# Performance work log

Measured on AMD Instinct MI355X. Metric: run time of the kernel, lower is better.

Reference implementation:

```python
import jax, jax.numpy as jnp
import numpy as np

N_OBJ, N_REL = 2048, 32768
OBJ_DIM, POOL, H, E, C = 4096, 2048, 512, 200, 151
GEO = 128
IMG_W, IMG_H = 1024.0, 768.0
NUM_ITER = 3


def _lin(x, W, b):
    return x @ W.T + b


def _gru(x, h, Wih, Whh, bih, bhh):
    # torch.nn.GRUCell math; gates stacked (r, z, n)
    gi = x @ Wih.T + bih
    gh = h @ Whh.T + bhh
    i_r, i_z, i_n = jnp.split(gi, 3, axis=-1)
    h_r, h_z, h_n = jnp.split(gh, 3, axis=-1)
    r = jax.nn.sigmoid(i_r + h_r)
    z = jax.nn.sigmoid(i_z + h_z)
    n = jnp.tanh(i_n + r * h_n)
    return (1.0 - z) * n + z * h


def _box_info(boxes, norm=None):
    # [x1,y1,x2,y2,cx,cy,w,h]
    wh = boxes[:, 2:4] - boxes[:, 0:2] + 1.0
    ctr = boxes[:, 0:2] + 0.5 * wh
    info = jnp.concatenate([boxes, ctr, wh], axis=1)
    return info / norm if norm is not None else info


def _box_pair_info(b1, b2):
    # b1,b2: [R,8] normalized box infos -> [R,32]
    ub = jnp.stack([jnp.minimum(b1[:, 0], b2[:, 0]), jnp.minimum(b1[:, 1], b2[:, 1]),
                    jnp.maximum(b1[:, 2], b2[:, 2]), jnp.maximum(b1[:, 3], b2[:, 3])], axis=1)
    ib = jnp.stack([jnp.maximum(b1[:, 0], b2[:, 0]), jnp.maximum(b1[:, 1], b2[:, 1]),
                    jnp.minimum(b1[:, 2], b2[:, 2]), jnp.minimum(b1[:, 3], b2[:, 3])], axis=1)
    inter = _box_info(ib)
    bad = (ib[:, 2] < ib[:, 0]) | (ib[:, 3] < ib[:, 1])
    inter = jnp.where(bad[:, None], 0.0, inter)
    return jnp.concatenate([b1, b2, _box_info(ub), inter], axis=1)


def _encode_box_info(boxes):
    # motifs 9-d geometry encoding
    wh = boxes[:, 2:4] - boxes[:, 0:2] + 1.0
    xy = boxes[:, 0:2] + 0.5 * wh
    w, h = wh[:, 0:1], wh[:, 1:2]
    x, y = xy[:, 0:1], xy[:, 1:2]
    x1, y1, x2, y2 = boxes[:, 0:1], boxes[:, 1:2], boxes[:, 2:3], boxes[:, 3:4]
    return jnp.concatenate([w / IMG_W, h / IMG_H, x / IMG_W, y / IMG_H, x1 / IMG_W,
                            y1 / IMG_H, x2 / IMG_W, y2 / IMG_H, w * h / (IMG_W * IMG_H)], axis=1)


def _forward(inst_roi_feats, union_features, boxes, emb_dist_W, emb_label_W, up_W, up_b,
             pairup_W, pairup_b, pos1_W, pos1_b, bn_g, bn_b, bn_m, bn_v, pos2_W, pos2_b,
             spt1_W, spt1_b, spt2_W, spt2_b, pairfin_W, pairfin_b, objhid_W, objhid_b,
             objfin_W, objfin_b, objU_W, objU_b, edgeU_W, edgeU_b,
             egru_Wih, egru_Whh, egru_bih, egru_bhh, ngru_Wih, ngru_Whh, ngru_bih, ngru_bhh,
             svw_W, svw_b, ovw_W, ovw_b, obj_labels, sub_idx, obj_idx):
    # ---- PairwiseFeatureExtractor ----
    # pos_embed: fc(9,32) -> eval BatchNorm1d(32) -> fc(32,128) -> ReLU
    p = _lin(_encode_box_info(boxes), pos1_W, pos1_b)
    p = (p - bn_m) * bn_g / jnp.sqrt(bn_v + 1e-5) + bn_b
    pos_embed = jax.nn.relu(_lin(p, pos2_W, pos2_b))
    emb_dist = emb_dist_W[obj_labels]                       # predcls: embed GT labels
    aug = _lin(jnp.concatenate([inst_roi_feats, emb_dist, pos_embed], 1), objhid_W, objhid_b)
    augment = jnp.concatenate([emb_label_W[obj_labels], inst_roi_feats, aug], 1)  # [N,4808]
    # pairwise (edge) features: gather head/tail reps + spatial gating
    obox = _box_info(boxes, norm=max(IMG_W, IMG_H, 100.0))  # [N,8]
    fused = _lin(augment, pairup_W, pairup_b).reshape(-1, 2, H)
    pair = jnp.concatenate([fused[:, 0][sub_idx], fused[:, 1][obj_idx]], 1)  # [R,1024]
    geo = _box_pair_info(obox[sub_idx], obox[obj_idx])      # [R,32]
    spt = jax.nn.relu(_lin(jax.nn.relu(_lin(geo, spt1_W, spt1_b)), spt2_W, spt2_b))
    rel_feats = jax.nn.relu(_lin(pair * spt, pairfin_W, pairfin_b))
    rel_feats = rel_feats + _lin(union_features, up_W, up_b)  # 'fusion' + dim-up
    obj_feats = jax.nn.relu(_lin(augment, objfin_W, objfin_b))
    # ---- IMP iterative message passing ----
    obj_rep = _lin(obj_feats, objU_W, objU_b)
    rel_rep = jax.nn.relu(_lin(rel_feats, edgeU_W, edgeU_b))
    vert = _gru(obj_rep, jnp.zeros_like(obj_rep), ngru_Wih, ngru_Whh, ngru_bih, ngru_bhh)
    edge = _gru(rel_rep, jnp.zeros_like(rel_rep), egru_Wih, egru_Whh, egru_bih, egru_bhh)
    n = vert.shape[0]
    for _ in range(NUM_ITER):
        sv, ov = vert[sub_idx], vert[obj_idx]
        ws = jax.nn.sigmoid(_lin(jnp.concatenate([sv, edge], 1), svw_W, svw_b))  # [R,1]
        wo = jax.nn.sigmoid(_lin(jnp.concatenate([ov, edge], 1), ovw_W, ovw_b))
        new_edge = _gru(ws * sv + wo * ov, edge, egru_Wih, egru_Whh, egru_bih, egru_bhh)
        # sub2rel @ (ws*edge) + obj2rel @ (wo*edge) == segment sums over pair indices
        ctx = jax.ops.segment_sum(ws * edge, sub_idx, n) + jax.ops.segment_sum(wo * edge, obj_idx, n)
        vert = _gru(ctx, vert, ngru_Wih, ngru_Whh, ngru_bih, ngru_bhh)
        edge = new_edge
    return vert, edge


def setup_inputs() -> dict:
    keys = jax.random.split(jax.random.key(0), 64)
    ki = iter(keys)

    def nrm(shape, s=0.02):
        return (jax.random.normal(next(ki), shape) * s).astype(jnp.float32)

    kb = jax.random.split(next(ki), 4)
    x1 = jax.random.uniform(kb[0], (N_OBJ,)) * (IMG_W - 200.0)
    y1 = jax.random.uniform(kb[1], (N_OBJ,)) * (IMG_H - 150.0)
    x2 = x1 + 1.0 + jax.random.uniform(kb[2], (N_OBJ,)) * 199.0
    y2 = y1 + 1.0 + jax.random.uniform(kb[3], (N_OBJ,)) * 149.0
    boxes = jnp.stack([x1, y1, x2, y2], axis=1).astype(jnp.float32)

    inp = {
        'inst_roi_feats': nrm((N_OBJ, OBJ_DIM), 1.0),
        'union_features': nrm((N_REL, OBJ_DIM), 1.0),
        'boxes': boxes,
        'emb_dist_W': nrm((C, E)), 'emb_label_W': nrm((C, E)),
        'up_W': nrm((POOL, OBJ_DIM)), 'up_b': jnp.zeros((POOL,), jnp.float32),
        'pairup_W': nrm((2 * H, H + OBJ_DIM + E)), 'pairup_b': jnp.zeros((2 * H,), jnp.float32),
        'pos1_W': nrm((32, 9)), 'pos1_b': jnp.zeros((32,), jnp.float32),
        'bn_g': jnp.ones((32,), jnp.float32), 'bn_b': jnp.zeros((32,), jnp.float32),
        'bn_m': nrm((32,)), 'bn_v': jnp.ones((32,), jnp.float32),
        'pos2_W': nrm((GEO, 32)), 'pos2_b': jnp.zeros((GEO,), jnp.float32),
        'spt1_W': nrm((H, 32)), 'spt1_b': jnp.zeros((H,), jnp.float32),
        'spt2_W': nrm((2 * H, H)), 'spt2_b': jnp.zeros((2 * H,), jnp.float32),
        'pairfin_W': nrm((POOL, 2 * H)), 'pairfin_b': jnp.zeros((POOL,), jnp.float32),
        'objhid_W': nrm((H, OBJ_DIM + E + GEO)), 'objhid_b': jnp.zeros((H,), jnp.float32),
        'objfin_W': nrm((POOL, H + OBJ_DIM + E)), 'objfin_b': jnp.zeros((POOL,), jnp.float32),
        'objU_W': nrm((H, POOL)), 'objU_b': jnp.zeros((H,), jnp.float32),
        'edgeU_W': nrm((H, POOL)), 'edgeU_b': jnp.zeros((H,), jnp.float32),
        'egru_Wih': nrm((3 * H, H)), 'egru_Whh': nrm((3 * H, H)),
        'egru_bih': jnp.zeros((3 * H,), jnp.float32), 'egru_bhh': jnp.zeros((3 * H,), jnp.float32),
        'ngru_Wih': nrm((3 * H, H)), 'ngru_Whh': nrm((3 * H, H)),
        'ngru_bih': jnp.zeros((3 * H,), jnp.float32), 'ngru_bhh': jnp.zeros((3 * H,), jnp.float32),
        'svw_W': nrm((1, 2 * H)), 'svw_b': jnp.zeros((1,), jnp.float32),
        'ovw_W': nrm((1, 2 * H)), 'ovw_b': jnp.zeros((1,), jnp.float32),
        'obj_labels': jax.random.randint(next(ki), (N_OBJ,), 0, C),
        'sub_idx': jax.random.randint(next(ki), (N_REL,), 0, N_OBJ),
        'obj_idx': jax.random.randint(next(ki), (N_REL,), 0, N_OBJ),
    }
    return inp


def reference(inst_roi_feats, union_features, boxes, emb_dist_W, emb_label_W, up_W, up_b,
              pairup_W, pairup_b, pos1_W, pos1_b, bn_g, bn_b, bn_m, bn_v, pos2_W, pos2_b,
              spt1_W, spt1_b, spt2_W, spt2_b, pairfin_W, pairfin_b, objhid_W, objhid_b,
              objfin_W, objfin_b, objU_W, objU_b, edgeU_W, edgeU_b,
              egru_Wih, egru_Whh, egru_bih, egru_bhh, ngru_Wih, ngru_Whh, ngru_bih, ngru_bhh,
              svw_W, svw_b, ovw_W, ovw_b, obj_labels, sub_idx, obj_idx):
    return _forward(inst_roi_feats, union_features, boxes, emb_dist_W, emb_label_W, up_W, up_b,
                    pairup_W, pairup_b, pos1_W, pos1_b, bn_g, bn_b, bn_m, bn_v, pos2_W, pos2_b,
                    spt1_W, spt1_b, spt2_W, spt2_b, pairfin_W, pairfin_b, objhid_W, objhid_b,
                    objfin_W, objfin_b, objU_W, objU_b, edgeU_W, edgeU_b,
                    egru_Wih, egru_Whh, egru_bih, egru_bhh, ngru_Wih, ngru_Whh, ngru_bih, ngru_bhh,
                    svw_W, svw_b, ovw_W, ovw_b, obj_labels, sub_idx, obj_idx)
```

## Files before the change

kernel.cpp:

```cpp
#include <hip/hip_runtime.h>
#include <stdint.h>

#define NOBJ 2048
#define NREL 32768

typedef __attribute__((ext_vector_type(8))) short short8;
typedef __attribute__((ext_vector_type(4))) float f32x4;
typedef __attribute__((ext_vector_type(4))) unsigned short ushort4v;

__device__ __forceinline__ unsigned short f2bs(float x){
  unsigned u = __float_as_uint(x);
  unsigned v = u + 0x7fffu + ((u >> 16) & 1u);
  return (unsigned short)(v >> 16);
}
__device__ __forceinline__ float b2f(unsigned short u){
  return __uint_as_float(((unsigned)u) << 16);
}
__device__ __forceinline__ float sigf(float x){ return 1.0f / (1.0f + expf(-x)); }

__device__ __forceinline__ void gload16(const unsigned short* g, unsigned short* l) {
  __builtin_amdgcn_global_load_lds(
      (const __attribute__((address_space(1))) unsigned int*)(uintptr_t)g,
      (__attribute__((address_space(3))) unsigned int*)(uintptr_t)l,
      16, 0, 0);
// ... 220 lines not shown
    asm volatile("" ::: "memory");
    __builtin_amdgcn_s_barrier();
    asm volatile("" ::: "memory");
    if (kt + 2 < NT) stage(cur, kt + 2);
  }

#pragma unroll
  for (int i = 0; i < 2; i++) {
#pragma unroll
    for (int j = 0; j < 2; j++) {
      const int col = n0 + wn + j * 16 + lrow;
      const float bv = bias[col];
#pragma unroll
      for (int q = 0; q < 4; q++) {
        const long row = m0 + wm + i * 16 + kg * 4 + q;
        float v = acc[i][j][q] + bv;
        if constexpr (RMODE == 1) v = fmaxf(v, 0.0f);
        C[row * (long)ldc + col] = f2bs(v);
      }
    }
  }
}


__global__ void cvt_pad4(const float* __restrict__ src, unsigned short* __restrict__ dst,
                         int rows, int K0, int Kp)
{
  const int kp4 = Kp >> 2;
  const long total = (long)rows * kp4;
  for (long i = blockIdx.x * (long)blockDim.x + threadIdx.x; i < total; i += (long)gridDim.x * blockDim.x) {
    int r = (int)(i / kp4), k = (int)(i - (long)r * kp4) << 2;
    ushort4v o;
    if (k < K0) {
      f32x4 v = *(const f32x4*)(src + (long)r * K0 + k);
      o[0] = f2bs(v[0]); o[1] = f2bs(v[1]); o[2] = f2bs(v[2]); o[3] = f2bs(v[3]);
    } else {
      o[0] = 0; o[1] = 0; o[2] = 0; o[3] = 0;
    }
    *(ushort4v*)(dst + (long)r * Kp + k) = o;
  }
}

struct CvtSeg { const float* src; unsigned short* dst; long base; long n4; };
struct Cvt9 { CvtSeg s[9]; long total; };

__global__ void cvt4_multi(Cvt9 cfg)
{
  for (long i = blockIdx.x * (long)blockDim.x + threadIdx.x; i < cfg.total;
       i += (long)gridDim.x * blockDim.x) {
#pragma unroll
    for (int k = 0; k < 9; k++) {
      if (i >= cfg.s[k].base && i < cfg.s[k].base + cfg.s[k].n4) {
        long j = i - cfg.s[k].base;
        f32x4 v = ((const f32x4*)cfg.s[k].src)[j];
        ushort4v o;
        o[0] = f2bs(v[0]); o[1] = f2bs(v[1]); o[2] = f2bs(v[2]); o[3] = f2bs(v[3]);
        ((ushort4v*)cfg.s[k].dst)[j] = o;
        break;
      }
    }
  }
}

__global__ void transpose_cvt(const float* __restrict__ src, unsigned short* __restrict__ dst,
                              int R, int C)
{
  __shared__ float tile[32][33];
  int c0 = blockIdx.x * 32, r0 = blockIdx.y * 32;
  for (int i = threadIdx.y; i < 32; i += 8)
    tile[i][threadIdx.x] = src[(long)(r0 + i) * C + c0 + threadIdx.x];
  __syncthreads();
  for (int i = threadIdx.y; i < 32; i += 8)
    dst[(long)(c0 + i) * R + r0 + threadIdx.x] = f2bs(tile[threadIdx.x][i]);
}

__global__ void comp_bias(const float* __restrict__ edgeU_W, const float* __restrict__ up_b,
                          const float* __restrict__ edgeU_b, float* __restrict__ b_comp)
{
  int j = (int)((blockIdx.x * (long)blockDim.x + threadIdx.x) >> 6);
  int l = threadIdx.x & 63;
  if (j >= 512) return;
  float s = 0.0f;
  for (int k = l; k < 2048; k += 64) s += edgeU_W[(long)j * 2048 + k] * up_b[k];
#pragma unroll
  for (int off = 32; off > 0; off >>= 1) s += __shfl_xor(s, off);
  if (l == 0) b_comp[j] = s + edgeU_b[j];
}

__global__ void bias_cat(const float* __restrict__ bhh, float* __restrict__ out)
{
  int j = blockIdx.x * blockDim.x + threadIdx.x;
  if (j < 3072) out[j] = (j < 1536) ? 0.0f : bhh[j - 1536];
}

__global__ void obox_k(const float* __restrict__ boxes, float* __restrict__ obox)
{
  int i = blockIdx.x * blockDim.x + threadIdx.x;
  if (i >= NOBJ) return;
  float x1 = boxes[i*4], y1 = boxes[i*4+1], x2 = boxes[i*4+2], y2 = boxes[i*4+3];
  float wdt = x2 - x1 + 1.0f, hgt = y2 - y1 + 1.0f;
  float cx = x1 + 0.5f * wdt, cy = y1 + 0.5f * hgt;
  const float inv = 1.0f / 1024.0f;
  float* o = obox + i * 8;
  o[0]=x1*inv; o[1]=y1*inv; o[2]=x2*inv; o[3]=y2*inv;
  o[4]=cx*inv; o[5]=cy*inv; o[6]=wdt*inv; o[7]=hgt*inv;
}

__global__ void posembed_k(const float* __restrict__ boxes,
                           const float* __restrict__ w1, const float* __restrict__ b1,
                           const float* __restrict__ g, const float* __restrict__ bb,
                           const float* __restrict__ mm, const float* __restrict__ vv,
                           const float* __restrict__ w2, const float* __restrict__ b2,
                           float* __restrict__ out)
{
  int o = blockIdx.x, t = threadIdx.x;
  __shared__ float e[9];
  __shared__ float p[32];
  if (t == 0) {
    float x1 = boxes[o*4], y1 = boxes[o*4+1], x2 = boxes[o*4+2], y2 = boxes[o*4+3];
    float wdt = x2 - x1 + 1.0f, hgt = y2 - y1 + 1.0f;
    float cx = x1 + 0.5f * wdt, cy = y1 + 0.5f * hgt;
    e[0]=wdt/1024.0f; e[1]=hgt/768.0f; e[2]=cx/1024.0f; e[3]=cy/768.0f;
    e[4]=x1/1024.0f;  e[5]=y1/768.0f;  e[6]=x2/1024.0f; e[7]=y2/768.0f;
    e[8]=wdt*hgt/(1024.0f*768.0f);
  }
  __syncthreads();
  if (t < 32) {
    float s = b1[t];
#pragma unroll
    for (int j = 0; j < 9; j++) s += w1[t*9+j] * e[j];
    s = (s - mm[t]) * g[t] / sqrtf(vv[t] + 1e-5f) + bb[t];
    p[t] = s;
  }
  __syncthreads();
  float s = b2[t];
#pragma unroll
  for (int j = 0; j < 32; j++) s += w2[t*32+j] * p[j];
  out[o*128 + t] = fmaxf(s, 0.0f);
}

__device__ __forceinline__ void pack8_store(unsigned short* dst, f32x4 a, f32x4 b)
{
  ushort4v o0, o1;
  o0[0]=f2bs(a[0]); o0[1]=f2bs(a[1]); o0[2]=f2bs(a[2]); o0[3]=f2bs(a[3]);
  o1[0]=f2bs(b[0]); o1[1]=f2bs(b[1]); o1[2]=f2bs(b[2]); o1[3]=f2bs(b[3]);
  *(ushort4v*)dst = o0;
  *(ushort4v*)(dst + 4) = o1;
}

__global__ void build_x1(const float* __restrict__ inst, const float* __restrict__ embd,
                         const int* __restrict__ labels, const float* __restrict__ pose,
                         unsigned short* __restrict__ X1b)
{
  const long total = (long)NOBJ * 560;
  for (long i = blockIdx.x * (long)blockDim.x + threadIdx.x; i < total; i += (long)gridDim.x * blockDim.x) {
    int r = (int)(i / 560), c = ((int)(i - (long)r * 560)) << 3;
    unsigned short* dst = X1b + (long)r * 4480 + c;
    const float* src;
    if (c < 4096)      src = inst + (long)r * 4096 + c;
    else if (c < 4296) src = embd + (long)labels[r] * 200 + (c - 4096);
    else if (c < 4424) src = pose + r * 128 + (c - 4296);
    else { ushort4v z = {0,0,0,0}; *(ushort4v*)dst = z; *(ushort4v*)(dst+4) = z; continue; }
    pack8_store(dst, *(const f32x4*)src, *((const f32x4*)src + 1));
  }
}

__global__ void build_aug(const float* __restrict__ embl, const int* __restrict__ labels,
                          const float* __restrict__ inst, unsigned short* __restrict__ augb)
{
  const long total = (long)NOBJ * 608;
  for (long i = blockIdx.x * (long)blockDim.x + threadIdx.x; i < total; i += (long)gridDim.x * blockDim.x) {
    int r = (int)(i / 608), c = ((int)(i - (long)r * 608)) << 3;
    if (c >= 4296 && c < 4808) continue;
    unsigned short* dst = augb + (long)r * 4864 + c;
    const float* src;
    if (c < 200)       src = embl + (long)labels[r] * 200 + c;
    else if (c < 4296) src = inst + (long)r * 4096 + (c - 200);
    else { ushort4v z = {0,0,0,0}; *(ushort4v*)dst = z; *(ushort4v*)(dst+4) = z; continue; }
    pack8_store(dst, *(const f32x4*)src, *((const f32x4*)src + 1));
  }
}

__global__ void build_geo(const float* __restrict__ obox, const int* __restrict__ sub,
                          const int* __restrict__ obj, unsigned short* __restrict__ geob)
{
  int r = blockIdx.x * blockDim.x + threadIdx.x;
  if (r >= NREL) return;
  const float* b1 = obox + sub[r] * 8;
  const float* b2 = obox + obj[r] * 8;
  float o[32];
#pragma unroll
  for (int j = 0; j < 8; j++) { o[j] = b1[j]; o[8+j] = b2[j]; }
  float ux1 = fminf(b1[0], b2[0]), uy1 = fminf(b1[1], b2[1]);
  float ux2 = fmaxf(b1[2], b2[2]), uy2 = fmaxf(b1[3], b2[3]);
  float uw = ux2 - ux1 + 1.0f, uh = uy2 - uy1 + 1.0f;
  o[16]=ux1; o[17]=uy1; o[18]=ux2; o[19]=uy2;
  o[20]=ux1+0.5f*uw; o[21]=uy1+0.5f*uh; o[22]=uw; o[23]=uh;
  float ix1 = fmaxf(b1[0], b2[0]), iy1 = fmaxf(b1[1], b2[1]);
  float ix2 = fminf(b1[2], b2[2]), iy2 = fminf(b1[3], b2[3]);
  bool bad = (ix2 < ix1) || (iy2 < iy1);
  float iw = ix2 - ix1 + 1.0f, ih = iy2 - iy1 + 1.0f;
  if (bad) {
#pragma unroll
    for (int j = 24; j < 32; j++) o[j] = 0.0f;
  } else {
    o[24]=ix1; o[25]=iy1; o[26]=ix2; o[27]=iy2;
    o[28]=ix1+0.5f*iw; o[29]=iy1+0.5f*ih; o[30]=iw; o[31]=ih;
  }
  unsigned short* gp = geob + (long)r * 64;
#pragma unroll
  for (int j = 0; j < 32; j++) gp[j] = f2bs(o[j]);
#pragma unroll
// ... 5 lines not shown
{
  const long total = (long)n * 64;
  for (long i = blockIdx.x * (long)blockDim.x + threadIdx.x; i < total; i += (long)gridDim.x * blockDim.x) {
    int r = (int)(i >> 6), c = ((int)(i & 63)) << 3;
    const unsigned short* gr = gi + (long)r * 1536;
    short8 vr = *(const short8*)(gr + c);
    short8 vz = *(const short8*)(gr + 512 + c);
    short8 vn = *(const short8*)(gr + 1024 + c);
    float hv[8];
#pragma unroll
    for (int k = 0; k < 8; k++) {
      float rr = sigf(b2f((unsigned short)vr[k]) + bhh[c + k]);
      float z  = sigf(b2f((unsigned short)vz[k]) + bhh[512 + c + k]);
      float nn = tanhf(b2f((unsigned short)vn[k]) + rr * bhh[1024 + c + k]);
      hv[k] = (1.0f - z) * nn;
    }
    float* hp = h + (long)r * 512 + c;
    *(f32x4*)hp = *(f32x4*)hv;
    *(f32x4*)(hp + 4) = *(f32x4*)(hv + 4);
    pack8_store(hb + (long)r * 512 + c, *(f32x4*)hv, *(f32x4*)(hv + 4));
  }
}

__global__ void gru_init_e(const unsigned short* __restrict__ gi, const float* __restrict__ bhh,
                           unsigned short* __restrict__ hb, int n)
{
  const long total = (long)n * 64;
  for (long i = blockIdx.x * (long)blockDim.x + threadIdx.x; i < total; i += (long)gridDim.x * blockDim.x) {
    int r = (int)(i >> 6), c = ((int)(i & 63)) << 3;
    const unsigned short* gr = gi + (long)r * 1536;
    short8 vr = *(const short8*)(gr + c);
    short8 vz = *(const short8*)(gr + 512 + c);
    short8 vn = *(const short8*)(gr + 1024 + c);
    float hv[8];
#pragma unroll
    for (int k = 0; k < 8; k++) {
      float rr = sigf(b2f((unsigned short)vr[k]) + bhh[c + k]);
      float z  = sigf(b2f((unsigned short)vz[k]) + bhh[512 + c + k]);
      float nn = tanhf(b2f((unsigned short)vn[k]) + rr * bhh[1024 + c + k]);
      hv[k] = (1.0f - z) * nn;
    }
    pack8_store(hb + (long)r * 512 + c, *(f32x4*)hv, *(f32x4*)(hv + 4));
  }
}

__global__ void gru_step_v(const unsigned short* __restrict__ gi, const unsigned short* __restrict__ gh,
                           int ghs, const float* __restrict__ hin, float* __restrict__ hout,
                           unsigned short* __restrict__ hb, int n)
{
  const long total = (long)n * 64;
  for (long i = blockIdx.x * (long)blockDim.x + threadIdx.x; i < total; i += (long)gridDim.x * blockDim.x) {
    int r = (int)(i >> 6), c = ((int)(i & 63)) << 3;
    const unsigned short* gr = gi + (long)r * 1536;
    const unsigned short* hr = gh + (long)r * ghs;
    short8 ir = *(const short8*)(gr + c);
    short8 iz = *(const short8*)(gr + 512 + c);
    short8 in_ = *(const short8*)(gr + 1024 + c);
    short8 hrr = *(const short8*)(hr + c);
    short8 hz = *(const short8*)(hr + 512 + c);
    short8 hn = *(const short8*)(hr + 1024 + c);
    const float* hi = hin + (long)r * 512 + c;
    f32x4 h0 = *(const f32x4*)hi;
    f32x4 h1 = *(const f32x4*)(hi + 4);
    float hv[8];
#pragma unroll
// ... 59 lines not shown
    float* fp = fout + (long)r * 512 + c;
    *(f32x4*)fp = *(f32x4*)hv;
    *(f32x4*)(fp + 4) = *(f32x4*)(hv + 4);
  }
  if (compute_w) {
    short8 svv = *(const short8*)(vertb + (long)s * 512 + c);
    short8 ovv = *(const short8*)(vertb + (long)o * 512 + c);
    float as = 0.0f, ao = 0.0f;
#pragma unroll
    for (int k = 0; k < 8; k++) {
      float e = hv[k];
      as += svwW[c + k] * b2f((unsigned short)svv[k]) + svwW[512 + c + k] * e;
      ao += ovwW[c + k] * b2f((unsigned short)ovv[k]) + ovwW[512 + c + k] * e;
    }
#pragma unroll
    for (int off = 32; off > 0; off >>= 1) {
      as += __shfl_xor(as, off);
      ao += __shfl_xor(ao, off);
    }
    if (l == 0) {
      ws_arr_out[r] = sigf(as + svwb[0]);
      wo_arr_out[r] = sigf(ao + ovwb[0]);
    }
  }
}

__global__ __launch_bounds__(256)
void edge_weights(const unsigned short* __restrict__ vertb, const unsigned short* __restrict__ edgeb,
                  const int* __restrict__ sub, const int* __restrict__ obj,
                  const float* __restrict__ svwW, const float* __restrict__ svwb,
                  const float* __restrict__ ovwW, const float* __restrict__ ovwb,
                  float* __restrict__ ws_arr, float* __restrict__ wo_arr)
{
  long gid = blockIdx.x * 256L + threadIdx.x;
  int r = (int)(gid >> 6);
  int l = (int)(gid & 63);
  if (r >= NREL) return;
  int s = sub[r], o = obj[r];
  const unsigned short* sv = vertb + (long)s * 512;
  const unsigned short* ov = vertb + (long)o * 512;
  const unsigned short* e  = edgeb + (long)r * 512;
  float as = 0.0f, ao = 0.0f;
#pragma unroll
  for (int k = 0; k < 8; k++) {
    int c = l + k * 64;
    float svv = b2f(sv[c]), ovv = b2f(ov[c]), ev = b2f(e[c]);
    as += svwW[c] * svv + svwW[512 + c] * ev;
    ao += ovwW[c] * ovv + ovwW[512 + c] * ev;
  }
#pragma unroll
  for (int off = 32; off > 0; off >>= 1) {
    as += __shfl_xor(as, off);
    ao += __shfl_xor(ao, off);
  }
  if (l == 0) {
    ws_arr[r] = sigf(as + svwb[0]);
    wo_arr[r] = sigf(ao + ovwb[0]);
  }
}


__global__ void csr_count(const int* __restrict__ sub, const int* __restrict__ obj,
                          int* __restrict__ cnt)
{
  int r = blockIdx.x * blockDim.x + threadIdx.x;
  if (r >= NREL) return;
  atomicAdd(&cnt[sub[r]], 1);
  atomicAdd(&cnt[obj[r]], 1);
}

__global__ __launch_bounds__(1024)
void csr_scan(const int* __restrict__ cnt, int* __restrict__ off)
{
  __shared__ int a[1024], b[1024];
  int t = threadIdx.x;
  int c0 = cnt[2*t], c1 = cnt[2*t+1];
  a[t] = c0 + c1;
  __syncthreads();
  int* src = a; int* dst = b;
  for (int s = 1; s < 1024; s <<= 1) {
// ... 128 lines not shown
    void* p = base + off;
    off += (bytes + 255) & ~(size_t)255;
    return p;
  };

  unsigned short* objhid_Wb  = (unsigned short*)alloc(512L  * 4480 * 2);
  unsigned short* pairup_Wb  = (unsigned short*)alloc(1024L * 4864 * 2);
  unsigned short* objfin_Wb  = (unsigned short*)alloc(2048L * 4864 * 2);
  unsigned short* up_Wtb     = (unsigned short*)alloc(4096L * 2048 * 2);
  unsigned short* pairfin_Wb = (unsigned short*)alloc(2048L * 1024 * 2);
  unsigned short* spt1_Wb    = (unsigned short*)alloc(512L  * 64   * 2);
  unsigned short* spt2_Wb    = (unsigned short*)alloc(1024L * 512  * 2);
  unsigned short* objU_Wb    = (unsigned short*)alloc(512L  * 2048 * 2);
  unsigned short* edgeU_Wb   = (unsigned short*)alloc(512L  * 2048 * 2);
  unsigned short* egru_Wihb  = (unsigned short*)alloc(1536L * 512  * 2);
  unsigned short* egru_Whhb  = (unsigned short*)alloc(1536L * 512  * 2);
  unsigned short* ngru_Wihb  = (unsigned short*)alloc(1536L * 512  * 2);
  unsigned short* vg_Wb      = (unsigned short*)alloc(3072L * 512  * 2);
  unsigned short* W_compb    = (unsigned short*)alloc(512L  * 4096 * 2);
  float*          b_comp     = (float*)alloc(512L * 4);
  float*          zbias      = (float*)alloc(4096L * 4);
  float*          vgbias     = (float*)alloc(3072L * 4);

  float*          obox      = (float*)alloc(NOBJ * 8L * 4);
  float*          pose      = (float*)alloc(NOBJ * 128L * 4);
  unsigned short* obj_featsb= (unsigned short*)alloc((long)NOBJ * 2048 * 2);
  unsigned short* obj_repb  = (unsigned short*)alloc((long)NOBJ * 512 * 2);
  unsigned short* giv       = (unsigned short*)alloc((long)NOBJ * 1536 * 2);
  unsigned short* VGb       = (unsigned short*)alloc((long)NOBJ * 3072 * 2);
  float*          vert      = (float*)alloc((long)NOBJ * 512 * 4);
  unsigned short* vertb     = (unsigned short*)alloc((long)NOBJ * 512 * 2);
  unsigned short* ctxb      = (unsigned short*)alloc((long)NOBJ * 512 * 2);
  unsigned short* geob      = (unsigned short*)alloc((long)NREL * 64 * 2);
  unsigned short* edgeb     = (unsigned short*)alloc((long)NREL * 512 * 2);
  float*          ws_arr    = (float*)alloc((long)NREL * 4);
  float*          wo_arr    = (float*)alloc((long)NREL * 4);

  int* cnt   = (int*)alloc(NOBJ * 4);
  int* coff  = (int*)alloc((NOBJ + 1) * 4);
  int* rcur  = (int*)alloc(NOBJ * 4);
  int* lists = (int*)alloc(2L * NREL * 4);

  char* regA = (char*)alloc((long)NREL * 512 * 4);
  unsigned short* X1b = (unsigned short*)regA;
  unsigned short* T1b = (unsigned short*)regA;
  char* regB = (char*)alloc((long)NOBJ * 4864 * 2 > (long)NREL * 512 * 2
                            ? (long)NOBJ * 4864 * 2 : (long)NREL * 512 * 2);
  unsigned short* augb     = (unsigned short*)regB;
  unsigned short* rel_repb = (unsigned short*)regB;
  unsigned short* fusedb = (unsigned short*)alloc((long)NOBJ * 1024 * 2);
  unsigned short* spt1b  = (unsigned short*)alloc((long)NREL * 512 * 2);
  char* big1 = (char*)alloc((long)NREL * 1536 * 4);
  unsigned short* G1    = (unsigned short*)big1;
  unsigned short* prodb = (unsigned short*)(big1 + (long)NREL * 1024 * 4);
  unsigned short* gi_e  = (unsigned short*)big1;
  unsigned short* GHb   = (unsigned short*)big1;

  float* d_out_vert = (float*)d_out;
  float* d_out_edge = (float*)d_out + (long)NOBJ * 512;

  cvt_pad4<<<nblk(512L*4480/4),  256, 0, stream>>>(objhid_W,  objhid_Wb,  512,  4424, 4480);
  cvt_pad4<<<nblk(1024L*4864/4), 256, 0, stream>>>(pairup_W,  pairup_Wb,  1024, 4808, 4864);
  cvt_pad4<<<nblk(2048L*4864/4), 256, 0, stream>>>(objfin_W,  objfin_Wb,  2048, 4808, 4864);
  cvt_pad4<<<nblk(512L*64/4),    256, 0, stream>>>(spt1_W,    spt1_Wb,    512,  32,   64);
  {
    Cvt9 cfg;
    long b = 0;
    auto seg = [&](int k, const float* s, unsigned short* d, long n4) {
      cfg.s[k].src = s; cfg.s[k].dst = d; cfg.s[k].base = b; cfg.s[k].n4 = n4; b += n4;
    };
    seg(0, pairfin_W, pairfin_Wb, 2048L*1024/4);
    seg(1, spt2_W,    spt2_Wb,    1024L*512/4);
    seg(2, objU_W,    objU_Wb,    512L*2048/4);
    seg(3, edgeU_W,   edgeU_Wb,   512L*2048/4);
    seg(4, egru_Wih,  egru_Wihb,  1536L*512/4);
    seg(5, egru_Whh,  egru_Whhb,  1536L*512/4);
    seg(6, ngru_Wih,  ngru_Wihb,  1536L*512/4);
    seg(7, egru_Wih,  vg_Wb,              1536L*512/4);
    seg(8, ngru_Whh,  vg_Wb + 1536L*512,  1536L*512/4);
    cfg.total = b;
    cvt4_multi<<<nblk(b), 256, 0, stream>>>(cfg);
  }
  bias_cat<<<12, 256, 0, stream>>>(ngru_bhh, vgbias);
  transpose_cvt<<<dim3(4096/32, 2048/32), dim3(32, 8), 0, stream>>>(up_W, up_Wtb, 2048, 4096);
  hipMemsetAsync(zbias, 0, 4096L * 4, stream);
  comp_bias<<<128, 256, 0, stream>>>(edgeU_W, up_b, edgeU_b, b_comp);
  G64(0, edgeU_Wb, up_Wtb, zbias, W_compb, 512, 4096, 2048, 2048, 4096);

  hipMemsetAsync(cnt, 0, NOBJ * 4, stream);
  hipMemsetAsync(rcur, 0, NOBJ * 4, stream);
  csr_count<<<NREL/256, 256, 0, stream>>>(sub, obj, cnt);
  csr_scan<<<1, 1024, 0, stream>>>(cnt, coff);
  csr_fill<<<NREL/256, 256, 0, stream>>>(sub, obj, coff, rcur, lists);

  obox_k<<<(NOBJ + 255) / 256, 256, 0, stream>>>(boxes, obox);
  posembed_k<<<NOBJ, 128, 0, stream>>>(boxes, pos1_W, pos1_b, bn_g, bn_b, bn_m, bn_v,
                                       pos2_W, pos2_b, pose);
  build_x1<<<nblk((long)NOBJ*560), 256, 0, stream>>>(inst, embd_W, labels, pose, X1b);
  build_aug<<<nblk((long)NOBJ*608), 256, 0, stream>>>(embl_W, labels, inst, augb);
  G64(0, X1b, objhid_Wb, objhid_b, augb + 4296, NOBJ, 512, 4480, 4480, 4864);
  G64(0, augb, pairup_Wb, pairup_b, fusedb, NOBJ, 1024, 4864, 4864, 1024);
  G64(1, augb, objfin_Wb, objfin_b, obj_featsb, NOBJ, 2048, 4864, 4864, 2048);
  G64(0, obj_featsb, objU_Wb, objU_b, obj_repb, NOBJ, 512, 2048, 2048, 512);
  G64(0, obj_repb, ngru_Wihb, ngru_bih, giv, NOBJ, 1536, 512, 512, 1536);
  gru_init_v<<<nblk((long)NOBJ*64), 256, 0, stream>>>(giv, ngru_bhh, vert, vertb, NOBJ);

  build_geo<<<(NREL + 255) / 256, 256, 0, stream>>>(obox, sub, obj, geob);
  GEMM(1,false,true ,false, dim3((NREL>>7)*(512>>7)),  geob, spt1_Wb, spt1_b, nullptr, spt1b, NREL, 512, 64, 64, 512, nullptr, nullptr, nullptr);
  GEMM(1,false,true ,true , dim3((NREL>>7)*(1024>>7)), spt1b, spt2_Wb, spt2_b, nullptr, prodb, NREL, 1024, 512, 512, 1024, fusedb, sub, obj);
  GEMM(1,false,true ,false, dim3((NREL>>7)*(2048>>7)), prodb, pairfin_Wb, pairfin_b, nullptr, G1, NREL, 2048, 1024, 1024, 2048, nullptr, nullptr, nullptr);
  GEMMF(0, dim3((NREL>>7)*(512>>7)), unionf, W_compb, b_comp, T1b, NREL, 512, 4096, 4096, 512);
  GEMMCB(2, dim3((NREL>>7)*(512>>7)), G1, edgeU_Wb, zbias, T1b, rel_repb, NREL, 512, 2048, 2048, 512);
  GEMM(0,false,true ,false, dim3((NREL>>7)*(1536>>7)), rel_repb, egru_Wihb, egru_bih, nullptr, gi_e, NREL, 1536, 512, 512, 1536, nullptr, nullptr, nullptr);
  gru_init_e<<<nblk((long)NREL*64), 256, 0, stream>>>(gi_e, egru_bhh, edgeb, NREL);

  edge_weights<<<NREL*64/256, 256, 0, stream>>>(vertb, edgeb, sub, obj,
                                                svw_W, svw_b, ovw_W, ovw_b, ws_arr, wo_arr);

  for (int it = 0; it < 3; it++) {
    const bool last = (it == 2);
    ctx_gather<<<NOBJ, 128, 0, stream>>>(edgeb, ws_arr, wo_arr, coff, lists, ctxb);
    G64(0, vertb, vg_Wb, vgbias, VGb, NOBJ, 3072, 512, 512, 3072);
    GEMM(0,false,true,false, dim3((NREL>>7)*(1536>>7)), edgeb, egru_Whhb, egru_bhh, nullptr, GHb, NREL, 1536, 512, 512, 1536, nullptr, nullptr, nullptr);
    G64(0, ctxb, ngru_Wihb, ngru_bih, giv, NOBJ, 1536, 512, 512, 1536);
    gru_step_v<<<nblk((long)NOBJ*64), 256, 0, stream>>>(giv, VGb + 1536, 3072, vert,
                                                        last ? d_out_vert : vert, vertb, NOBJ);
    gru_step_e2<<<NREL*64/256, 256, 0, stream>>>(GHb, VGb, ws_arr, wo_arr, ws_arr, wo_arr,
                                                 sub, obj, egru_bih, edgeb,
                                                 last ? d_out_edge : nullptr, vertb,
                                                 svw_W, svw_b, ovw_W, ovw_b,
                                                 last ? 0 : 1, NREL);
  }
}
```

Measured before the change: 1.672 ms.

## Merge small launches: dual-GEMM kernel, unified conversions, fused edge init and weights

Adds a gemm64_dual kernel that runs two independent GEMMs sharing M and K in one launch, used for pairup+objfin and for the per-iteration vert/ctx GEMMs. It also folds the weight conversions into one multi-segment kernel, merges build_x1/build_aug, computes box info inline in build_geo, and fuses gru_init_e with edge_weights. Memsets are merged or replaced by a bias kernel. The aim is to cut kernel launch count and the small-kernel tails. In exchange, the dual GEMM picks its operands at runtime instead of through template constants, which may cost a little inside each tile.

Measured after the change: 1.663 ms. No clear change (-0.6%).

```diff
diff --git a/kernel.cpp b/kernel.cpp
--- a/kernel.cpp
+++ b/kernel.cpp
@@ -266,40 +266,137 @@
   }
 }
 
-
-__global__ void cvt_pad4(const float* __restrict__ src, unsigned short* __restrict__ dst,
-                         int rows, int K0, int Kp)
-{
-  const int kp4 = Kp >> 2;
-  const long total = (long)rows * kp4;
-  for (long i = blockIdx.x * (long)blockDim.x + threadIdx.x; i < total; i += (long)gridDim.x * blockDim.x) {
-    int r = (int)(i / kp4), k = (int)(i - (long)r * kp4) << 2;
-    ushort4v o;
-    if (k < K0) {
-      f32x4 v = *(const f32x4*)(src + (long)r * K0 + k);
-      o[0] = f2bs(v[0]); o[1] = f2bs(v[1]); o[2] = f2bs(v[2]); o[3] = f2bs(v[3]);
-    } else {
-      o[0] = 0; o[1] = 0; o[2] = 0; o[3] = 0;
-    }
-    *(ushort4v*)(dst + (long)r * Kp + k) = o;
-  }
-}
-
-struct CvtSeg { const float* src; unsigned short* dst; long base; long n4; };
-struct Cvt9 { CvtSeg s[9]; long total; };
-
-__global__ void cvt4_multi(Cvt9 cfg)
+__global__ __launch_bounds__(256, 4)
+void gemm64_dual(const unsigned short* __restrict__ A1, const unsigned short* __restrict__ B1,
+                 const float* __restrict__ bias1, unsigned short* __restrict__ C1,
+                 int N1, int ldc1, int rmode1,
+                 const unsigned short* __restrict__ A2, const unsigned short* __restrict__ B2,
+                 const float* __restrict__ bias2, unsigned short* __restrict__ C2,
+                 int N2, int ldc2, int rmode2,
+                 int M, int K, int lda)
+{
+  __shared__ __align__(16) unsigned short As[2][64 * 64];
+  __shared__ __align__(16) unsigned short Bs[2][64 * 64];
+  const int t = threadIdx.x;
+  const int lane = t & 63;
+  const int w = t >> 6;
+  const int nwg = gridDim.x;
+  const int q8 = nwg >> 3, r8 = nwg & 7;
+  const int xcd = blockIdx.x & 7, bidx = blockIdx.x >> 3;
+  const int wgid = (xcd < r8 ? xcd * (q8 + 1) : r8 * (q8 + 1) + (xcd - r8) * q8) + bidx;
+
+  const int nt1 = (M >> 6) * (N1 >> 6);
+  const unsigned short* A; const unsigned short* B;
+  const float* bias; unsigned short* C;
+  int N, ldc, rmode, tile;
+  if (wgid < nt1) { A = A1; B = B1; bias = bias1; C = C1; N = N1; ldc = ldc1; rmode = rmode1; tile = wgid; }
+  else            { A = A2; B = B2; bias = bias2; C = C2; N = N2; ldc = ldc2; rmode = rmode2; tile = wgid - nt1; }
+
+  const int ntile = N >> 6;
+  const int bm = tile / ntile, bn = tile - bm * ntile;
+  const int m0 = bm << 6, n0 = bn << 6;
+  const int wm = (w & 1) << 5, wn = (w >> 1) << 5;
+  const int lrow = lane & 15, kg = lane >> 4;
+  const int rx = lrow & 7;
+
+  const int srow8 = lane >> 3;
+  const int sslot = ((lane & 7) ^ srow8) << 3;
+  const unsigned short* Ag = A + (long)(m0 + w * 16 + srow8) * lda + sslot;
+  const unsigned short* Bg = B + (long)(n0 + w * 16 + srow8) * K + sslot;
+  const long lda8 = 8L * lda, ldb8 = 8L * K;
+  const int NT = K >> 6;
+
+  auto stage = [&](int buf, int kt) {
+    const unsigned short* a_ = Ag + (long)kt * 64;
+    const unsigned short* b_ = Bg + (long)kt * 64;
+    gload16(a_,        As[buf] + (w * 16) * 64);
+    gload16(a_ + lda8, As[buf] + (w * 16 + 8) * 64);
+    gload16(b_,        Bs[buf] + (w * 16) * 64);
+    gload16(b_ + ldb8, Bs[buf] + (w * 16 + 8) * 64);
+  };
+
+  f32x4 acc[2][2] = {};
+
+  stage(0, 0);
+  if (NT > 1) stage(1, 1);
+
+  for (int kt = 0; kt < NT; ++kt) {
+    const int cur = kt & 1;
+    if (kt + 1 < NT) asm volatile("s_waitcnt vmcnt(4)" ::: "memory");
+    else             asm volatile("s_waitcnt vmcnt(0)" ::: "memory");
+    __builtin_amdgcn_s_barrier();
+    asm volatile("" ::: "memory");
+
+    const unsigned short* As_ = As[cur];
+    const unsigned short* Bs_ = Bs[cur];
+    short8 afr[2][2], bfr[2][2];
+#pragma unroll
+    for (int i = 0; i < 2; i++) {
+      const int ra = wm + i * 16 + lrow;
+#pragma unroll
+      for (int ks = 0; ks < 2; ks++)
+        afr[i][ks] = *(const short8*)(As_ + ra * 64 + (((ks * 4 + kg) ^ rx) << 3));
+    }
+#pragma unroll
+    for (int j = 0; j < 2; j++) {
+      const int rb = wn + j * 16 + lrow;
+#pragma unroll
+      for (int ks = 0; ks < 2; ks++)
+        bfr[j][ks] = *(const short8*)(Bs_ + rb * 64 + (((ks * 4 + kg) ^ rx) << 3));
+    }
+#pragma unroll
+    for (int i = 0; i < 2; i++)
+#pragma unroll
+      for (int j = 0; j < 2; j++)
+#pragma unroll
+        for (int ks = 0; ks < 2; ks++)
+          acc[i][j] = __builtin_amdgcn_mfma_f32_16x16x32_bf16(afr[i][ks], bfr[j][ks], acc[i][j], 0, 0, 0);
+    asm volatile("" ::: "memory");
+    __builtin_amdgcn_s_barrier();
+    asm volatile("" ::: "memory");
+    if (kt + 2 < NT) stage(cur, kt + 2);
+  }
+
+#pragma unroll
+  for (int i = 0; i < 2; i++) {
+#pragma unroll
+    for (int j = 0; j < 2; j++) {
+      const int col = n0 + wn + j * 16 + lrow;
+      const float bv = bias[col];
+#pragma unroll
+      for (int q = 0; q < 4; q++) {
+        const long row = m0 + wm + i * 16 + kg * 4 + q;
+        float v = acc[i][j][q] + bv;
+        if (rmode == 1) v = fmaxf(v, 0.0f);
+        C[row * (long)ldc + col] = f2bs(v);
+      }
+    }
+  }
+}
+
+
+struct SegC { const float* src; unsigned short* dst; long base; long nq; int k0q; int kpq; };
+struct Cvt13 { SegC s[13]; long total; };
+
+__global__ void cvt_all(Cvt13 cfg)
 {
   for (long i = blockIdx.x * (long)blockDim.x + threadIdx.x; i < cfg.total;
        i += (long)gridDim.x * blockDim.x) {
 #pragma unroll
-    for (int k = 0; k < 9; k++) {
-      if (i >= cfg.s[k].base && i < cfg.s[k].base + cfg.s[k].n4) {
-        long j = i - cfg.s[k].base;
-        f32x4 v = ((const f32x4*)cfg.s[k].src)[j];
+    for (int k = 0; k < 13; k++) {
+      if (i >= cfg.s[k].base && i < cfg.s[k].base + cfg.s[k].nq) {
+        long q = i - cfg.s[k].base;
+        int kpq = cfg.s[k].kpq, k0q = cfg.s[k].k0q;
+        long r = q / kpq;
+        int kq = (int)(q - r * kpq);
         ushort4v o;
-        o[0] = f2bs(v[0]); o[1] = f2bs(v[1]); o[2] = f2bs(v[2]); o[3] = f2bs(v[3]);
-        ((ushort4v*)cfg.s[k].dst)[j] = o;
+        if (kq < k0q) {
+          f32x4 v = *(const f32x4*)(cfg.s[k].src + r * (long)(k0q << 2) + (kq << 2));
+          o[0] = f2bs(v[0]); o[1] = f2bs(v[1]); o[2] = f2bs(v[2]); o[3] = f2bs(v[3]);
+        } else {
+          o[0] = 0; o[1] = 0; o[2] = 0; o[3] = 0;
+        }
+        *(ushort4v*)(cfg.s[k].dst + r * (long)(kpq << 2) + (kq << 2)) = o;
         break;
       }
     }
@@ -331,23 +428,12 @@
   if (l == 0) b_comp[j] = s + edgeU_b[j];
 }
 
-__global__ void bias_cat(const float* __restrict__ bhh, float* __restrict__ out)
+__global__ void bias_misc(const float* __restrict__ bhh, float* __restrict__ vgbias,
+                          float* __restrict__ zbias)
 {
   int j = blockIdx.x * blockDim.x + threadIdx.x;
-  if (j < 3072) out[j] = (j < 1536) ? 0.0f : bhh[j - 1536];
-}
-
-__global__ void obox_k(const float* __restrict__ boxes, float* __restrict__ obox)
-{
-  int i = blockIdx.x * blockDim.x + threadIdx.x;
-  if (i >= NOBJ) return;
-  float x1 = boxes[i*4], y1 = boxes[i*4+1], x2 = boxes[i*4+2], y2 = boxes[i*4+3];
-  float wdt = x2 - x1 + 1.0f, hgt = y2 - y1 + 1.0f;
-  float cx = x1 + 0.5f * wdt, cy = y1 + 0.5f * hgt;
-  const float inv = 1.0f / 1024.0f;
-  float* o = obox + i * 8;
-  o[0]=x1*inv; o[1]=y1*inv; o[2]=x2*inv; o[3]=y2*inv;
-  o[4]=cx*inv; o[5]=cy*inv; o[6]=wdt*inv; o[7]=hgt*inv;
+  if (j < 3072) vgbias[j] = (j < 1536) ? 0.0f : bhh[j - 1536];
+  if (j < 4096) zbias[j] = 0.0f;
 }
 
 __global__ void posembed_k(const float* __restrict__ boxes,
@@ -392,46 +478,55 @@
   *(ushort4v*)(dst + 4) = o1;
 }
 
-__global__ void build_x1(const float* __restrict__ inst, const float* __restrict__ embd,
-                         const int* __restrict__ labels, const float* __restrict__ pose,
-                         unsigned short* __restrict__ X1b)
-{
-  const long total = (long)NOBJ * 560;
+__global__ void build_feed(const float* __restrict__ inst, const float* __restrict__ embd,
+                           const float* __restrict__ embl, const int* __restrict__ labels,
+                           const float* __restrict__ pose,
+                           unsigned short* __restrict__ X1b, unsigned short* __restrict__ augb)
+{
+  const long T1n = (long)NOBJ * 560;
+  const long total = T1n + (long)NOBJ * 608;
   for (long i = blockIdx.x * (long)blockDim.x + threadIdx.x; i < total; i += (long)gridDim.x * blockDim.x) {
-    int r = (int)(i / 560), c = ((int)(i - (long)r * 560)) << 3;
-    unsigned short* dst = X1b + (long)r * 4480 + c;
-    const float* src;
-    if (c < 4096)      src = inst + (long)r * 4096 + c;
-    else if (c < 4296) src = embd + (long)labels[r] * 200 + (c - 4096);
-    else if (c < 4424) src = pose + r * 128 + (c - 4296);
-    else { ushort4v z = {0,0,0,0}; *(ushort4v*)dst = z; *(ushort4v*)(dst+4) = z; continue; }
-    pack8_store(dst, *(const f32x4*)src, *((const f32x4*)src + 1));
-  }
-}
-
-__global__ void build_aug(const float* __restrict__ embl, const int* __restrict__ labels,
-                          const float* __restrict__ inst, unsigned short* __restrict__ augb)
-{
-  const long total = (long)NOBJ * 608;
-  for (long i = blockIdx.x * (long)blockDim.x + threadIdx.x; i < total; i += (long)gridDim.x * blockDim.x) {
-    int r = (int)(i / 608), c = ((int)(i - (long)r * 608)) << 3;
-    if (c >= 4296 && c < 4808) continue;
-    unsigned short* dst = augb + (long)r * 4864 + c;
-    const float* src;
-    if (c < 200)       src = embl + (long)labels[r] * 200 + c;
-    else if (c < 4296) src = inst + (long)r * 4096 + (c - 200);
-    else { ushort4v z = {0,0,0,0}; *(ushort4v*)dst = z; *(ushort4v*)(dst+4) = z; continue; }
-    pack8_store(dst, *(const f32x4*)src, *((const f32x4*)src + 1));
-  }
-}
-
-__global__ void build_geo(const float* __restrict__ obox, const int* __restrict__ sub,
+    if (i < T1n) {
+      int r = (int)(i / 560), c = ((int)(i - (long)r * 560)) << 3;
+      unsigned short* dst = X1b + (long)r * 4480 + c;
+      const float* src;
+      if (c < 4096)      src = inst + (long)r * 4096 + c;
+      else if (c < 4296) src = embd + (long)labels[r] * 200 + (c - 4096);
+      else if (c < 4424) src = pose + r * 128 + (c - 4296);
+      else { ushort4v z = {0,0,0,0}; *(ushort4v*)dst = z; *(ushort4v*)(dst+4) = z; continue; }
+      pack8_store(dst, *(const f32x4*)src, *((const f32x4*)src + 1));
+    } else {
+      long ii = i - T1n;
+      int r = (int)(ii / 608), c = ((int)(ii - (long)r * 608)) << 3;
+      if (c >= 4296 && c < 4808) continue;
+      unsigned short* dst = augb + (long)r * 4864 + c;
+      const float* src;
+      if (c < 200)       src = embl + (long)labels[r] * 200 + c;
+      else if (c < 4296) src = inst + (long)r * 4096 + (c - 200);
+      else { ushort4v z = {0,0,0,0}; *(ushort4v*)dst = z; *(ushort4v*)(dst+4) = z; continue; }
+      pack8_store(dst, *(const f32x4*)src, *((const f32x4*)src + 1));
+    }
+  }
+}
+
+__device__ __forceinline__ void boxinfo8(const float* __restrict__ bx, float* o)
+{
+  float x1 = bx[0], y1 = bx[1], x2 = bx[2], y2 = bx[3];
+  float wdt = x2 - x1 + 1.0f, hgt = y2 - y1 + 1.0f;
+  float cx = x1 + 0.5f * wdt, cy = y1 + 0.5f * hgt;
+  const float inv = 1.0f / 1024.0f;
+  o[0]=x1*inv; o[1]=y1*inv; o[2]=x2*inv; o[3]=y2*inv;
+  o[4]=cx*inv; o[5]=cy*inv; o[6]=wdt*inv; o[7]=hgt*inv;
+}
+
+__global__ void build_geo(const float* __restrict__ boxes, const int* __restrict__ sub,
                           const int* __restrict__ obj, unsigned short* __restrict__ geob)
 {
   int r = blockIdx.x * blockDim.x + threadIdx.x;
   if (r >= NREL) return;
-  const float* b1 = obox + sub[r] * 8;
-  const float* b2 = obox + obj[r] * 8;
+  float b1[8], b2[8];
+  boxinfo8(boxes + sub[r] * 4, b1);
+  boxinfo8(boxes + obj[r] * 4, b2);
   float o[32];
 #pragma unroll
   for (int j = 0; j < 8; j++) { o[j] = b1[j]; o[8+j] = b2[j]; }
@@ -483,25 +578,51 @@
   }
 }
 
-__global__ void gru_init_e(const unsigned short* __restrict__ gi, const float* __restrict__ bhh,
-                           unsigned short* __restrict__ hb, int n)
-{
-  const long total = (long)n * 64;
-  for (long i = blockIdx.x * (long)blockDim.x + threadIdx.x; i < total; i += (long)gridDim.x * blockDim.x) {
-    int r = (int)(i >> 6), c = ((int)(i & 63)) << 3;
-    const unsigned short* gr = gi + (long)r * 1536;
-    short8 vr = *(const short8*)(gr + c);
-    short8 vz = *(const short8*)(gr + 512 + c);
-    short8 vn = *(const short8*)(gr + 1024 + c);
-    float hv[8];
-#pragma unroll
-    for (int k = 0; k < 8; k++) {
-      float rr = sigf(b2f((unsigned short)vr[k]) + bhh[c + k]);
-      float z  = sigf(b2f((unsigned short)vz[k]) + bhh[512 + c + k]);
-      float nn = tanhf(b2f((unsigned short)vn[k]) + rr * bhh[1024 + c + k]);
-      hv[k] = (1.0f - z) * nn;
-    }
-    pack8_store(hb + (long)r * 512 + c, *(f32x4*)hv, *(f32x4*)(hv + 4));
+__global__ __launch_bounds__(256)
+void gru_init_e_w(const unsigned short* __restrict__ gi, const float* __restrict__ bhh,
+                  unsigned short* __restrict__ edgeb,
+                  const unsigned short* __restrict__ vertb,
+                  const int* __restrict__ sub, const int* __restrict__ obj,
+                  const float* __restrict__ svwW, const float* __restrict__ svwb,
+                  const float* __restrict__ ovwW, const float* __restrict__ ovwb,
+                  float* __restrict__ ws_arr, float* __restrict__ wo_arr, int n)
+{
+  long gid = blockIdx.x * 256L + threadIdx.x;
+  int r = (int)(gid >> 6);
+  int l = (int)(gid & 63);
+  if (r >= n) return;
+  const int c = l << 3;
+  const unsigned short* gr = gi + (long)r * 1536;
+  short8 vr = *(const short8*)(gr + c);
+  short8 vz = *(const short8*)(gr + 512 + c);
+  short8 vn = *(const short8*)(gr + 1024 + c);
+  float hv[8];
+#pragma unroll
+  for (int k = 0; k < 8; k++) {
+    float rr = sigf(b2f((unsigned short)vr[k]) + bhh[c + k]);
+    float z  = sigf(b2f((unsigned short)vz[k]) + bhh[512 + c + k]);
+    float nn = tanhf(b2f((unsigned short)vn[k]) + rr * bhh[1024 + c + k]);
+    hv[k] = (1.0f - z) * nn;
+  }
+  pack8_store(edgeb + (long)r * 512 + c, *(f32x4*)hv, *(f32x4*)(hv + 4));
+  int s = sub[r], o = obj[r];
+  short8 svv = *(const short8*)(vertb + (long)s * 512 + c);
+  short8 ovv = *(const short8*)(vertb + (long)o * 512 + c);
+  float as = 0.0f, ao = 0.0f;
+#pragma unroll
+  for (int k = 0; k < 8; k++) {
+    float e = hv[k];
+    as += svwW[c + k] * b2f((unsigned short)svv[k]) + svwW[512 + c + k] * e;
+    ao += ovwW[c + k] * b2f((unsigned short)ovv[k]) + ovwW[512 + c + k] * e;
+  }
+#pragma unroll
+  for (int off = 32; off > 0; off >>= 1) {
+    as += __shfl_xor(as, off);
+    ao += __shfl_xor(ao, off);
+  }
+  if (l == 0) {
+    ws_arr[r] = sigf(as + svwb[0]);
+    wo_arr[r] = sigf(ao + ovwb[0]);
   }
 }
 
@@ -607,40 +728,6 @@
       ws_arr_out[r] = sigf(as + svwb[0]);
       wo_arr_out[r] = sigf(ao + ovwb[0]);
     }
-  }
-}
-
-__global__ __launch_bounds__(256)
-void edge_weights(const unsigned short* __restrict__ vertb, const unsigned short* __restrict__ edgeb,
-                  const int* __restrict__ sub, const int* __restrict__ obj,
-                  const float* __restrict__ svwW, const float* __restrict__ svwb,
-                  const float* __restrict__ ovwW, const float* __restrict__ ovwb,
-                  float* __restrict__ ws_arr, float* __restrict__ wo_arr)
-{
-  long gid = blockIdx.x * 256L + threadIdx.x;
-  int r = (int)(gid >> 6);
-  int l = (int)(gid & 63);
-  if (r >= NREL) return;
-  int s = sub[r], o = obj[r];
-  const unsigned short* sv = vertb + (long)s * 512;
-  const unsigned short* ov = vertb + (long)o * 512;
-  const unsigned short* e  = edgeb + (long)r * 512;
-  float as = 0.0f, ao = 0.0f;
-#pragma unroll
-  for (int k = 0; k < 8; k++) {
-    int c = l + k * 64;
-    float svv = b2f(sv[c]), ovv = b2f(ov[c]), ev = b2f(e[c]);
-    as += svwW[c] * svv + svwW[512 + c] * ev;
-    ao += ovwW[c] * ovv + ovwW[512 + c] * ev;
-  }
-#pragma unroll
-  for (int off = 32; off > 0; off >>= 1) {
-    as += __shfl_xor(as, off);
-    ao += __shfl_xor(ao, off);
-  }
-  if (l == 0) {
-    ws_arr[r] = sigf(as + svwb[0]);
-    wo_arr[r] = sigf(ao + ovwb[0]);
   }
 }
 
@@ -815,7 +902,6 @@
   float*          zbias      = (float*)alloc(4096L * 4);
   float*          vgbias     = (float*)alloc(3072L * 4);
 
-  float*          obox      = (float*)alloc(NOBJ * 8L * 4);
   float*          pose      = (float*)alloc(NOBJ * 128L * 4);
   unsigned short* obj_featsb= (unsigned short*)alloc((long)NOBJ * 2048 * 2);
   unsigned short* obj_repb  = (unsigned short*)alloc((long)NOBJ * 512 * 2);
@@ -830,8 +916,8 @@
   float*          wo_arr    = (float*)alloc((long)NREL * 4);
 
   int* cnt   = (int*)alloc(NOBJ * 4);
+  int* rcur  = (int*)alloc(NOBJ * 4);
   int* coff  = (int*)alloc((NOBJ + 1) * 4);
-  int* rcur  = (int*)alloc(NOBJ * 4);
   int* lists = (int*)alloc(2L * NREL * 4);
 
   char* regA = (char*)alloc((long)NREL * 512 * 4);
@@ -852,70 +938,72 @@
   float* d_out_vert = (float*)d_out;
   float* d_out_edge = (float*)d_out + (long)NOBJ * 512;
 
-  cvt_pad4<<<nblk(512L*4480/4),  256, 0, stream>>>(objhid_W,  objhid_Wb,  512,  4424, 4480);
-  cvt_pad4<<<nblk(1024L*4864/4), 256, 0, stream>>>(pairup_W,  pairup_Wb,  1024, 4808, 4864);
-  cvt_pad4<<<nblk(2048L*4864/4), 256, 0, stream>>>(objfin_W,  objfin_Wb,  2048, 4808, 4864);
-  cvt_pad4<<<nblk(512L*64/4),    256, 0, stream>>>(spt1_W,    spt1_Wb,    512,  32,   64);
   {
-    Cvt9 cfg;
+    Cvt13 cfg;
     long b = 0;
-    auto seg = [&](int k, const float* s, unsigned short* d, long n4) {
-      cfg.s[k].src = s; cfg.s[k].dst = d; cfg.s[k].base = b; cfg.s[k].n4 = n4; b += n4;
+    auto seg = [&](int k, const float* s, unsigned short* d, long rows, int K0, int Kp) {
+      cfg.s[k].src = s; cfg.s[k].dst = d; cfg.s[k].base = b;
+      cfg.s[k].k0q = K0 >> 2; cfg.s[k].kpq = Kp >> 2;
+      cfg.s[k].nq = rows * (long)(Kp >> 2);
+      b += cfg.s[k].nq;
     };
-    seg(0, pairfin_W, pairfin_Wb, 2048L*1024/4);
-    seg(1, spt2_W,    spt2_Wb,    1024L*512/4);
-    seg(2, objU_W,    objU_Wb,    512L*2048/4);
-    seg(3, edgeU_W,   edgeU_Wb,   512L*2048/4);
-    seg(4, egru_Wih,  egru_Wihb,  1536L*512/4);
-    seg(5, egru_Whh,  egru_Whhb,  1536L*512/4);
-    seg(6, ngru_Wih,  ngru_Wihb,  1536L*512/4);
-    seg(7, egru_Wih,  vg_Wb,              1536L*512/4);
-    seg(8, ngru_Whh,  vg_Wb + 1536L*512,  1536L*512/4);
+    seg(0,  objhid_W,  objhid_Wb,  512,  4424, 4480);
+    seg(1,  pairup_W,  pairup_Wb,  1024, 4808, 4864);
+    seg(2,  objfin_W,  objfin_Wb,  2048, 4808, 4864);
+    seg(3,  spt1_W,    spt1_Wb,    512,  32,   64);
+    seg(4,  pairfin_W, pairfin_Wb, 2048, 1024, 1024);
+    seg(5,  spt2_W,    spt2_Wb,    1024, 512,  512);
+    seg(6,  objU_W,    objU_Wb,    512,  2048, 2048);
+    seg(7,  edgeU_W,   edgeU_Wb,   512,  2048, 2048);
+    seg(8,  egru_Wih,  egru_Wihb,  1536, 512,  512);
+    seg(9,  egru_Whh,  egru_Whhb,  1536, 512,  512);
+    seg(10, ngru_Wih,  ngru_Wihb,  1536, 512,  512);
+    seg(11, egru_Wih,  vg_Wb,              1536, 512, 512);
+    seg(12, ngru_Whh,  vg_Wb + 1536L*512,  1536, 512, 512);
     cfg.total = b;
-    cvt4_multi<<<nblk(b), 256, 0, stream>>>(cfg);
-  }
-  bias_cat<<<12, 256, 0, stream>>>(ngru_bhh, vgbias);
+    cvt_all<<<nblk(b), 256, 0, stream>>>(cfg);
+  }
+  bias_misc<<<16, 256, 0, stream>>>(ngru_bhh, vgbias, zbias);
   transpose_cvt<<<dim3(4096/32, 2048/32), dim3(32, 8), 0, stream>>>(up_W, up_Wtb, 2048, 4096);
-  hipMemsetAsync(zbias, 0, 4096L * 4, stream);
   comp_bias<<<128, 256, 0, stream>>>(edgeU_W, up_b, edgeU_b, b_comp);
   G64(0, edgeU_Wb, up_Wtb, zbias, W_compb, 512, 4096, 2048, 2048, 4096);
 
-  hipMemsetAsync(cnt, 0, NOBJ * 4, stream);
-  hipMemsetAsync(rcur, 0, NOBJ * 4, stream);
+  hipMemsetAsync(cnt, 0, 2L * NOBJ * 4, stream);
   csr_count<<<NREL/256, 256, 0, stream>>>(sub, obj, cnt);
   csr_scan<<<1, 1024, 0, stream>>>(cnt, coff);
   csr_fill<<<NREL/256, 256, 0, stream>>>(sub, obj, coff, rcur, lists);
 
-  obox_k<<<(NOBJ + 255) / 256, 256, 0, stream>>>(boxes, obox);
   posembed_k<<<NOBJ, 128, 0, stream>>>(boxes, pos1_W, pos1_b, bn_g, bn_b, bn_m, bn_v,
                                        pos2_W, pos2_b, pose);
-  build_x1<<<nblk((long)NOBJ*560), 256, 0, stream>>>(inst, embd_W, labels, pose, X1b);
-  build_aug<<<nblk((long)NOBJ*608), 256, 0, stream>>>(embl_W, labels, inst, augb);
+  build_feed<<<nblk((long)NOBJ*(560+608)), 256, 0, stream>>>(inst, embd_W, embl_W, labels, pose,
+                                                             X1b, augb);
   G64(0, X1b, objhid_Wb, objhid_b, augb + 4296, NOBJ, 512, 4480, 4480, 4864);
-  G64(0, augb, pairup_Wb, pairup_b, fusedb, NOBJ, 1024, 4864, 4864, 1024);
-  G64(1, augb, objfin_Wb, objfin_b, obj_featsb, NOBJ, 2048, 4864, 4864, 2048);
+  gemm64_dual<<<dim3((NOBJ>>6)*((1024+2048)>>6)), 256, 0, stream>>>(
+      augb, pairup_Wb, pairup_b, fusedb,     1024, 1024, 0,
+      augb, objfin_Wb, objfin_b, obj_featsb, 2048, 2048, 1,
+      NOBJ, 4864, 4864);
   G64(0, obj_featsb, objU_Wb, objU_b, obj_repb, NOBJ, 512, 2048, 2048, 512);
   G64(0, obj_repb, ngru_Wihb, ngru_bih, giv, NOBJ, 1536, 512, 512, 1536);
   gru_init_v<<<nblk((long)NOBJ*64), 256, 0, stream>>>(giv, ngru_bhh, vert, vertb, NOBJ);
 
-  build_geo<<<(NREL + 255) / 256, 256, 0, stream>>>(obox, sub, obj, geob);
+  build_geo<<<(NREL + 255) / 256, 256, 0, stream>>>(boxes, sub, obj, geob);
   GEMM(1,false,true ,false, dim3((NREL>>7)*(512>>7)),  geob, spt1_Wb, spt1_b, nullptr, spt1b, NREL, 512, 64, 64, 512, nullptr, nullptr, nullptr);
   GEMM(1,false,true ,true , dim3((NREL>>7)*(1024>>7)), spt1b, spt2_Wb, spt2_b, nullptr, prodb, NREL, 1024, 512, 512, 1024, fusedb, sub, obj);
   GEMM(1,false,true ,false, dim3((NREL>>7)*(2048>>7)), prodb, pairfin_Wb, pairfin_b, nullptr, G1, NREL, 2048, 1024, 1024, 2048, nullptr, nullptr, nullptr);
   GEMMF(0, dim3((NREL>>7)*(512>>7)), unionf, W_compb, b_comp, T1b, NREL, 512, 4096, 4096, 512);
   GEMMCB(2, dim3((NREL>>7)*(512>>7)), G1, edgeU_Wb, zbias, T1b, rel_repb, NREL, 512, 2048, 2048, 512);
   GEMM(0,false,true ,false, dim3((NREL>>7)*(1536>>7)), rel_repb, egru_Wihb, egru_bih, nullptr, gi_e, NREL, 1536, 512, 512, 1536, nullptr, nullptr, nullptr);
-  gru_init_e<<<nblk((long)NREL*64), 256, 0, stream>>>(gi_e, egru_bhh, edgeb, NREL);
-
-  edge_weights<<<NREL*64/256, 256, 0, stream>>>(vertb, edgeb, sub, obj,
-                                                svw_W, svw_b, ovw_W, ovw_b, ws_arr, wo_arr);
+  gru_init_e_w<<<NREL*64/256, 256, 0, stream>>>(gi_e, egru_bhh, edgeb, vertb, sub, obj,
+                                                svw_W, svw_b, ovw_W, ovw_b, ws_arr, wo_arr, NREL);
 
   for (int it = 0; it < 3; it++) {
     const bool last = (it == 2);
     ctx_gather<<<NOBJ, 128, 0, stream>>>(edgeb, ws_arr, wo_arr, coff, lists, ctxb);
-    G64(0, vertb, vg_Wb, vgbias, VGb, NOBJ, 3072, 512, 512, 3072);
+    gemm64_dual<<<dim3((NOBJ>>6)*((3072+1536)>>6)), 256, 0, stream>>>(
+        vertb, vg_Wb,     vgbias,   VGb, 3072, 3072, 0,
+        ctxb,  ngru_Wihb, ngru_bih, giv, 1536, 1536, 0,
+        NOBJ, 512, 512);
     GEMM(0,false,true,false, dim3((NREL>>7)*(1536>>7)), edgeb, egru_Whhb, egru_bhh, nullptr, GHb, NREL, 1536, 512, 512, 1536, nullptr, nullptr, nullptr);
-    G64(0, ctxb, ngru_Wihb, ngru_bih, giv, NOBJ, 1536, 512, 512, 1536);
     gru_step_v<<<nblk((long)NOBJ*64), 256, 0, stream>>>(giv, VGb + 1536, 3072, vert,
                                                         last ? d_out_vert : vert, vertb, NOBJ);
     gru_step_e2<<<NREL*64/256, 256, 0, stream>>>(GHb, VGb, ws_arr, wo_arr, ws_arr, wo_arr,
```
